# Kernel optimization log

Measured on AMD Instinct MI355X. Metric: run time of the kernel, lower is better.

Reference implementation:

```python
import jax, jax.numpy as jnp
import numpy as np

HIDDEN_DIM = 256
CLIP_LEN = 2
B, NQ, T, D = 64, 10, 2048, 256


def setup_inputs() -> dict:
    key = jax.random.key(0)
    ks = jax.random.split(key, 10)
    s = 1.0 / np.sqrt(HIDDEN_DIM)  # torch GRU/Linear init scale
    return {
        "pred_logits": jax.random.normal(ks[0], (B, NQ, 2), jnp.float32),
        "pred_spans": jax.random.uniform(ks[1], (B, NQ, 2), jnp.float32),
        "memory": jax.random.normal(ks[2], (B, T, D), jnp.float32),
        "src_vid": jax.random.normal(ks[3], (B, T, D), jnp.float32),
        "W_ih": jax.random.normal(ks[4], (3 * D, D), jnp.float32) * s,
        "W_hh": jax.random.normal(ks[5], (3 * D, D), jnp.float32) * s,
        "b_ih": jax.random.normal(ks[6], (3 * D,), jnp.float32) * s,
        "b_hh": jax.random.normal(ks[7], (3 * D,), jnp.float32) * s,
        "W_sal": jax.random.normal(ks[8], (D, D), jnp.float32) * s,
        "b_sal": jax.random.normal(ks[9], (D,), jnp.float32) * s,
    }


def _gru_last_hidden(x, W_ih, W_hh, b_ih, b_hh):
    # x: [B, T, D] -> final hidden state [B, D] (torch nn.GRU, h0 = 0)
    b, t, d = x.shape
    gi = jnp.einsum("btd,gd->btg", x, W_ih) + b_ih  # [B, T, 3D], precompute input gates

    def step(h, gi_t):
        gh = jnp.einsum("bd,gd->bg", h, W_hh) + b_hh
        ir, iz, inn = jnp.split(gi_t, 3, axis=-1)
        hr, hz, hn = jnp.split(gh, 3, axis=-1)
        r = jax.nn.sigmoid(ir + hr)
        z = jax.nn.sigmoid(iz + hz)
        n = jnp.tanh(inn + r * hn)
        h_new = (1.0 - z) * n + z * h
        return h_new, None

    h0 = jnp.zeros((b, d), x.dtype)
    hT, _ = jax.lax.scan(step, h0, jnp.swapaxes(gi, 0, 1))
    return hT


def reference(pred_logits, pred_spans, memory, src_vid, W_ih, W_hh, b_ih, b_hh, W_sal, b_sal):
    b, t, d = memory.shape
    # top-1 span selection (sort descending, take first == argmax of class-0 prob)
    scores = jax.nn.softmax(pred_logits, axis=-1)[..., 0]  # [B, NQ]
    best = jnp.argmax(scores, axis=-1)  # [B]
    span = jnp.take_along_axis(pred_spans, best[:, None, None], axis=1)[:, 0, :]  # [B, 2] (cx, w)
    cx, w = span[:, 0], span[:, 1]
    xx = jnp.stack([cx - 0.5 * w, cx + 0.5 * w], axis=-1) * (t * CLIP_LEN)
    se = jnp.floor(xx / CLIP_LEN).astype(jnp.int32)  # [B, 2] start/end frame indices
    start = jnp.clip(se[:, 0], 0, t - 1)
    end_eff = jnp.minimum(se[:, 1], t - 1)
    # on-device dynamic slice + zero pad to fixed length T (replaces python loop)
    idx = start[:, None] + jnp.arange(t)[None, :]  # [B, T]
    valid = idx <= end_eff[:, None]  # empty slice if end < start
    idx_c = jnp.clip(idx, 0, t - 1)
    sliced = jnp.take_along_axis(src_vid, idx_c[..., None], axis=1) * valid[..., None].astype(src_vid.dtype)
    # GRU over padded slice, take last hidden
    hidden = _gru_last_hidden(sliced, W_ih, W_hh, b_ih, b_hh)  # [B, D]
    weight = jnp.einsum("bd,btd->bt", hidden, src_vid)  # [B, T]
    mem = memory * weight[..., None] + memory
    proj = jnp.einsum("btd,ed->bte", mem, W_sal) + b_sal
    saliency = jnp.sum(proj, axis=-1) / np.sqrt(HIDDEN_DIM)
    return saliency  # [B, T]
```

## Files before the change

kernel.cpp:

```cpp
#include <hip/hip_runtime.h>
#include <hip/hip_bf16.h>
#include <stdint.h>

#define T_SEQ 2048
#define DDIM 256
#define G3 768
#define NB 64
#define NQR 10

typedef _Float16 h2f __attribute__((ext_vector_type(2)));
typedef _Float16 f16x8 __attribute__((ext_vector_type(8)));
typedef float f32x4 __attribute__((ext_vector_type(4)));
typedef unsigned u32x4 __attribute__((ext_vector_type(4)));

__device__ __forceinline__ float fdot2u(unsigned a, unsigned b, float c) {
    return __builtin_amdgcn_fdot2(__builtin_bit_cast(h2f, a),
                                  __builtin_bit_cast(h2f, b), c, false);
}
__device__ __forceinline__ unsigned packf16(float a, float b) {
    auto p = __builtin_amdgcn_cvt_pkrtz(a, b);
    return __builtin_bit_cast(unsigned, p);
}
__device__ __forceinline__ float unpk(unsigned u, int hi) {
    h2f p = __builtin_bit_cast(h2f, u);
    return hi ? (float)p[1] : (float)p[0];
}
__device__ __forceinline__ float sigmf(float x) { return 1.0f / (1.0f + __expf(-x)); }
__device__ __forceinline__ float tanhff(float x) {
    float ax = fabsf(x);
    float e = __expf(2.0f * ax);
    float t = 1.0f - 2.0f / (e + 1.0f);
    return copysignf(t, x);
}

__global__ __launch_bounds__(256) void k_prologue(
    const float* __restrict__ logits, const float* __restrict__ spans,
    const float* __restrict__ W_sal, const float* __restrict__ b_sal,
    int* __restrict__ meta, float* __restrict__ wcol, float* __restrict__ bsum) {
    int tid = threadIdx.x;
    if (tid < NB) {
        int b = tid;
        float bestv = -1e30f; int best = 0;
        for (int q = 0; q < NQR; ++q) {
            float l0 = logits[(b * NQR + q) * 2 + 0];
            float l1 = logits[(b * NQR + q) * 2 + 1];
            float sc = sigmf(l0 - l1);
            if (sc > bestv) { bestv = sc; best = q; }
        }
        float cx = spans[(b * NQR + best) * 2 + 0];
        float w  = spans[(b * NQR + best) * 2 + 1];
        float x0 = (cx - 0.5f * w) * (float)(T_SEQ * 2);
        float x1 = (cx + 0.5f * w) * (float)(T_SEQ * 2);
        int se0 = (int)floorf(x0 * 0.5f);
        int se1 = (int)floorf(x1 * 0.5f);
        int start = min(max(se0, 0), T_SEQ - 1);
        int end_eff = min(se1, T_SEQ - 1);
        int len = end_eff - start + 1;
        if (len < 0) len = 0;
        meta[b] = start; meta[NB + b] = len;
    }
    float acc = 0.f;
    for (int e = 0; e < DDIM; ++e) acc += W_sal[e * DDIM + tid];
    wcol[tid] = acc;
    if (tid < 64) {
        float p = b_sal[tid] + b_sal[tid + 64] + b_sal[tid + 128] + b_sal[tid + 192];
        for (int off = 32; off; off >>= 1) p += __shfl_down(p, off, 64);
        if (tid == 0) *bsum = p;
    }
}

__global__ __launch_bounds__(256) void k_prep(
    const float* __restrict__ W_hh, unsigned* __restrict__ w4) {
    int g = blockIdx.x, k = threadIdx.x;
    if (k < 128) {
        unsigned v = packf16(W_hh[g * DDIM + 2 * k], W_hh[g * DDIM + 2 * k + 1]);
        w4[((k >> 2) * G3 + g) * 4 + (k & 3)] = v;
    }
}

__global__ __launch_bounds__(256) void k_prepI(
    const float* __restrict__ W_ih, unsigned* __restrict__ wfragI) {
    int u = blockIdx.x * 256 + threadIdx.x;
    int jj = u & 3;
    int l  = (u >> 2) & 63;
    int kc = (u >> 8) & 7;
    int ct = u >> 11;
    int col = ct * 16 + (l & 15);
    int k = kc * 32 + ((l >> 4) << 3) + jj * 2;
    wfragI[u] = packf16(W_ih[col * DDIM + k], W_ih[col * DDIM + k + 1]);
}

__global__ __launch_bounds__(512, 2) void k_gemm(
    const float* __restrict__ src_vid, const unsigned* __restrict__ wfragI,
    const float* __restrict__ b_ih, const int* __restrict__ meta,
    unsigned* __restrict__ gi2, int t0, int tc, int TC) {
    int b = blockIdx.y;
    int len = meta[NB + b];
    int start = meta[b];
    int tbase = t0 + blockIdx.x * 256;
    int tend = t0 + tc; if (tend > len) tend = len;
    int tcap = tbase + 256; if (tend > tcap) tend = tcap;
    if (tbase >= tend) return;

    int tid = threadIdx.x, lane = tid & 63, w = tid >> 6;

    u32x4 bfr[6][8];
    const u32x4* wf = (const u32x4*)wfragI;
#pragma unroll
    for (int j = 0; j < 6; ++j)
#pragma unroll
        for (int kc = 0; kc < 8; ++kc)
            bfr[j][kc] = wf[((w * 6 + j) * 8 + kc) * 64 + lane];

    int row = lane & 15, kg = lane >> 4;
    float bv[6];
#pragma unroll
    for (int j = 0; j < 6; ++j) bv[j] = b_ih[(w * 6 + j) * 16 + row];

    __shared__ unsigned As[2048];
    int sr = tid >> 5, sx = tid & 31;

    for (int tch = tbase; tch < tend; tch += 16) {
        int tr = tch + sr;
        u32x4 pk = {0u, 0u, 0u, 0u};
        if (tr < len) {
            const float* sp = src_vid + ((size_t)b * T_SEQ + start + tr) * DDIM + sx * 8;
            float4 a0 = *(const float4*)sp;
            float4 a1 = *(const float4*)(sp + 4);
            pk[0] = packf16(a0.x, a0.y); pk[1] = packf16(a0.z, a0.w);
            pk[2] = packf16(a1.x, a1.y); pk[3] = packf16(a1.z, a1.w);
        }
        *(u32x4*)&As[sr * 128 + ((sx ^ sr) << 2)] = pk;
        __syncthreads();

        f32x4 d[6];
#pragma unroll
        for (int j = 0; j < 6; ++j) d[j] = (f32x4){bv[j], bv[j], bv[j], bv[j]};
#pragma unroll
        for (int kc = 0; kc < 8; ++kc) {
            u32x4 av = *(const u32x4*)&As[row * 128 + (((kc * 4 + kg) ^ row) << 2)];
            f16x8 af = __builtin_bit_cast(f16x8, av);
#pragma unroll
            for (int j = 0; j < 6; ++j)
                d[j] = __builtin_amdgcn_mfma_f32_16x16x32_f16(
                    af, __builtin_bit_cast(f16x8, bfr[j][kc]), d[j], 0, 0, 0);
        }

#pragma unroll
        for (int j = 0; j < 6; ++j) {
            int cflat = (w * 6 + j) * 16 + row;
            int gate = cflat >> 8;
            int pairi = (cflat & 255) >> 1;
#pragma unroll
            for (int reg = 0; reg < 4; ++reg) {
                int t = tch + kg * 4 + reg;
                float v = d[j][reg];
                float o = __shfl_xor(v, 1, 64);
                if (!(lane & 1) && t < tend)
                    gi2[((size_t)b * TC + (t - t0)) * 384 + gate * 128 + pairi] =
                        packf16(v, o);
            }
        }
        __syncthreads();
    }
}

__global__ void __launch_bounds__(512, 2) k_gru(
    const unsigned* __restrict__ gi2, const unsigned* __restrict__ w4,
    const float* __restrict__ b_ih, const float* __restrict__ b_hh,
    const int* __restrict__ meta, float* __restrict__ h_state,
    int t0, int t1, int TC) {
    int b = blockIdx.x, tid = threadIdx.x;
    int c = tid & 255, half = tid >> 8;
    int len = meta[NB + b];

    u32x4 wrq[16], wzq[16], wnq[16];
    const u32x4* w4v = (const u32x4*)w4;
    const u32x4* wb = w4v + (size_t)(half * 16) * G3;
#pragma unroll
    for (int q = 0; q < 16; ++q) {
        wrq[q] = wb[q * G3 + c];
        wzq[q] = wb[q * G3 + 256 + c];
        wnq[q] = wb[q * G3 + 512 + c];
    }

    float bhR = (half == 0) ? b_hh[c] : 0.f;
    float bhZ = (half == 0) ? b_hh[256 + c] : 0.f;
    float bhN = (half == 0) ? b_hh[512 + c] : 0.f;
    float biR = b_ih[c], biZ = b_ih[256 + c], biN = b_ih[512 + c];

    __shared__ unsigned hl[128];
    __shared__ float pl[3][256];

    float h = 0.f;
    if (half == 0) {
        if (t0 != 0) h = h_state[b * DDIM + c];
        float hp = __shfl_xor(h, 1, 64);
        if (!(c & 1)) hl[c >> 1] = packf16(h, hp);
    }

    const unsigned* gb2 = gi2 + (size_t)b * TC * 384 + (c >> 1);
    int sel = c & 1;
    float gR = biR, gZ = biZ, gN = biN;
    if (half == 0 && t0 < t1 && t0 < len) {
        gR = unpk(gb2[0], sel); gZ = unpk(gb2[128], sel); gN = unpk(gb2[256], sel);
    }
    __syncthreads();

    for (int t = t0; t < t1; ++t) {
        float nR = biR, nZ = biZ, nN = biN;
        int tn = t + 1;
        if (half == 0 && tn < t1 && tn < len) {
            const unsigned* gp = gb2 + (size_t)(tn - t0) * 384;
            nR = unpk(gp[0], sel); nZ = unpk(gp[128], sel); nN = unpk(gp[256], sel);
        }
        float r0 = bhR, z0 = bhZ, n0 = bhN, r1 = 0.f, z1 = 0.f, n1 = 0.f;
        const u32x4* hb = (const u32x4*)hl + half * 16;
#pragma unroll
        for (int q = 0; q < 16; ++q) {
            u32x4 h4 = hb[q];
            r0 = fdot2u(h4.x, wrq[q].x, r0);
            z0 = fdot2u(h4.x, wzq[q].x, z0);
            n0 = fdot2u(h4.x, wnq[q].x, n0);
            r1 = fdot2u(h4.y, wrq[q].y, r1);
            z1 = fdot2u(h4.y, wzq[q].y, z1);
            n1 = fdot2u(h4.y, wnq[q].y, n1);
            r0 = fdot2u(h4.z, wrq[q].z, r0);
            z0 = fdot2u(h4.z, wzq[q].z, z0);
            n0 = fdot2u(h4.z, wnq[q].z, n0);
            r1 = fdot2u(h4.w, wrq[q].w, r1);
            z1 = fdot2u(h4.w, wzq[q].w, z1);
            n1 = fdot2u(h4.w, wnq[q].w, n1);
        }
        float hr = r0 + r1, hz = z0 + z1, hn = n0 + n1;
        if (half == 1) {
            pl[0][c] = hr; pl[1][c] = hz; pl[2][c] = hn;
        }
        __syncthreads();
        if (half == 0) {
            hr += pl[0][c]; hz += pl[1][c]; hn += pl[2][c];
            float r = sigmf(gR + hr);
            float z = sigmf(gZ + hz);
            float n = tanhff(gN + r * hn);
            h = (1.0f - z) * n + z * h;
            float hp = __shfl_xor(h, 1, 64);
            if (!(c & 1)) hl[c >> 1] = packf16(h, hp);
        }
        gR = nR; gZ = nZ; gN = nN;
        __syncthreads();
    }
    if (half == 0) h_state[b * DDIM + c] = h;
}

__global__ __launch_bounds__(256) void k_epi(
    const float* __restrict__ memory, const float* __restrict__ src_vid,
    const float* __restrict__ h_state, const float* __restrict__ wcol,
    const float* __restrict__ bsum, float* __restrict__ out) {
    int wid = blockIdx.x * 4 + (threadIdx.x >> 6);
    int lane = threadIdx.x & 63;
    int b = wid >> 11;
    int t = wid & 2047;
    const float4* mp = (const float4*)(memory + ((size_t)b * T_SEQ + t) * DDIM);
    const float4* sp = (const float4*)(src_vid + ((size_t)b * T_SEQ + t) * DDIM);
    const float4* hp = (const float4*)(h_state + b * DDIM);
    const float4* wp = (const float4*)wcol;
    float4 m = mp[lane], s = sp[lane], hv = hp[lane], wc = wp[lane];
    float s1 = m.x * wc.x + m.y * wc.y + m.z * wc.z + m.w * wc.w;
    float s2 = hv.x * s.x + hv.y * s.y + hv.z * s.z + hv.w * s.w;
    for (int off = 32; off; off >>= 1) {
        s1 += __shfl_down(s1, off, 64);
        s2 += __shfl_down(s2, off, 64);
    }
    if (lane == 0) out[(size_t)b * T_SEQ + t] = ((1.0f + s2) * s1 + *bsum) * 0.0625f;
}

extern "C" void kernel_launch(void* const* d_in, const int* in_sizes, int n_in,
                              void* d_out, int out_size, void* d_ws, size_t ws_size,
                              hipStream_t stream) {
    const float* logits  = (const float*)d_in[0];
    const float* spans   = (const float*)d_in[1];
    const float* memory  = (const float*)d_in[2];
    const float* src_vid = (const float*)d_in[3];
    const float* W_ih    = (const float*)d_in[4];
    const float* W_hh    = (const float*)d_in[5];
    const float* b_ih    = (const float*)d_in[6];
    const float* b_hh    = (const float*)d_in[7];
    const float* W_sal   = (const float*)d_in[8];
    const float* b_sal   = (const float*)d_in[9];
    float* out = (float*)d_out;
    char* ws = (char*)d_ws;

    const size_t OFF_META = 0;
    const size_t OFF_WCOL = 1024;
    const size_t OFF_BSUM = 2048;
    const size_t OFF_H    = 4096;
    const size_t OFF_W4   = 69632;
    const size_t OFF_WFI  = 462848;
    const size_t OFF_GI   = 856064;

    int* meta       = (int*)(ws + OFF_META);
    float* wcol     = (float*)(ws + OFF_WCOL);
    float* bsum     = (float*)(ws + OFF_BSUM);
    float* h_state  = (float*)(ws + OFF_H);
    unsigned* w4    = (unsigned*)(ws + OFF_W4);
    unsigned* wfragI= (unsigned*)(ws + OFF_WFI);
    unsigned* gi2   = (unsigned*)(ws + OFF_GI);

    size_t gi_cap = (ws_size > OFF_GI) ? (ws_size - OFF_GI) : 0;
    long long tc_max = (long long)(gi_cap / ((size_t)NB * 384 * 4));
    int TC = (tc_max > T_SEQ) ? T_SEQ : (int)tc_max;
    if (TC < 16) TC = 16;

    k_prologue<<<dim3(1), dim3(256), 0, stream>>>(logits, spans, W_sal, b_sal, meta, wcol, bsum);
    k_prep<<<dim3(G3), dim3(256), 0, stream>>>(W_hh, w4);
    k_prepI<<<dim3(384), dim3(256), 0, stream>>>(W_ih, wfragI);
    for (int t0 = 0; t0 < T_SEQ; t0 += TC) {
        int tc = T_SEQ - t0; if (tc > TC) tc = TC;
        k_gemm<<<dim3((tc + 255) / 256, NB), dim3(512), 0, stream>>>(
            src_vid, wfragI, b_ih, meta, gi2, t0, tc, TC);
        k_gru<<<dim3(NB), dim3(512), 0, stream>>>(
            gi2, w4, b_ih, b_hh, meta, h_state, t0, t0 + tc, TC);
    }
    k_epi<<<dim3(NB * T_SEQ / 4), dim3(256), 0, stream>>>(
        memory, src_vid, h_state, wcol, bsum, out);
}
```

Measured before the change: 2.572 ms.

## Split GRU recurrence K-dimension over four thread groups and fold biases into gates

The GRU recurrent kernel now runs 1024 threads per batch row, splitting the 256-wide hidden dot products across four K-quarters instead of two. Each thread holds only 24 weight vectors instead of 48, and three of the groups reduce their partial sums through shared memory. Input and hidden biases for the r and z gates are pre-combined in the prologue and folded into the input-gate GEMM output, with packed biases used for padded timesteps. The aim is a shorter per-step serial dot-product chain and lower register pressure on the latency-bound recurrence, at the cost of more shared-memory traffic and a larger block per step.

Measured after the change: 2.992 ms. 1.16x slower.

```diff
diff --git a/kernel.cpp b/kernel.cpp
--- a/kernel.cpp
+++ b/kernel.cpp
@@ -36,7 +36,9 @@
 __global__ __launch_bounds__(256) void k_prologue(
     const float* __restrict__ logits, const float* __restrict__ spans,
     const float* __restrict__ W_sal, const float* __restrict__ b_sal,
-    int* __restrict__ meta, float* __restrict__ wcol, float* __restrict__ bsum) {
+    const float* __restrict__ b_ih, const float* __restrict__ b_hh,
+    int* __restrict__ meta, float* __restrict__ wcol, float* __restrict__ bsum,
+    float* __restrict__ bias_comb, unsigned* __restrict__ biasp) {
     int tid = threadIdx.x;
     if (tid < NB) {
         int b = tid;
@@ -67,6 +69,17 @@
         for (int off = 32; off; off >>= 1) p += __shfl_down(p, off, 64);
         if (tid == 0) *bsum = p;
     }
+#pragma unroll
+    for (int r = 0; r < 3; ++r) {
+        int g = tid + r * 256;
+        bias_comb[g] = b_ih[g] + (g < 512 ? b_hh[g] : 0.f);
+    }
+    __syncthreads();
+#pragma unroll
+    for (int r = 0; r < 2; ++r) {
+        int p = tid + r * 256;
+        if (p < 384) biasp[p] = packf16(bias_comb[2 * p], bias_comb[2 * p + 1]);
+    }
 }
 
 __global__ __launch_bounds__(256) void k_prep(
@@ -92,7 +105,7 @@
 
 __global__ __launch_bounds__(512, 2) void k_gemm(
     const float* __restrict__ src_vid, const unsigned* __restrict__ wfragI,
-    const float* __restrict__ b_ih, const int* __restrict__ meta,
+    const float* __restrict__ bias_comb, const int* __restrict__ meta,
     unsigned* __restrict__ gi2, int t0, int tc, int TC) {
     int b = blockIdx.y;
     int len = meta[NB + b];
@@ -115,7 +128,7 @@
     int row = lane & 15, kg = lane >> 4;
     float bv[6];
 #pragma unroll
-    for (int j = 0; j < 6; ++j) bv[j] = b_ih[(w * 6 + j) * 16 + row];
+    for (int j = 0; j < 6; ++j) bv[j] = bias_comb[(w * 6 + j) * 16 + row];
 
     __shared__ unsigned As[2048];
     int sr = tid >> 5, sx = tid & 31;
@@ -165,35 +178,33 @@
     }
 }
 
-__global__ void __launch_bounds__(512, 2) k_gru(
+__global__ void __launch_bounds__(1024) k_gru(
     const unsigned* __restrict__ gi2, const unsigned* __restrict__ w4,
-    const float* __restrict__ b_ih, const float* __restrict__ b_hh,
+    const unsigned* __restrict__ biasp, const float* __restrict__ b_hh,
     const int* __restrict__ meta, float* __restrict__ h_state,
     int t0, int t1, int TC) {
     int b = blockIdx.x, tid = threadIdx.x;
-    int c = tid & 255, half = tid >> 8;
+    int c = tid & 255, kq = tid >> 8;
     int len = meta[NB + b];
 
-    u32x4 wrq[16], wzq[16], wnq[16];
+    u32x4 wq[8][3];
     const u32x4* w4v = (const u32x4*)w4;
-    const u32x4* wb = w4v + (size_t)(half * 16) * G3;
-#pragma unroll
-    for (int q = 0; q < 16; ++q) {
-        wrq[q] = wb[q * G3 + c];
-        wzq[q] = wb[q * G3 + 256 + c];
-        wnq[q] = wb[q * G3 + 512 + c];
-    }
-
-    float bhR = (half == 0) ? b_hh[c] : 0.f;
-    float bhZ = (half == 0) ? b_hh[256 + c] : 0.f;
-    float bhN = (half == 0) ? b_hh[512 + c] : 0.f;
-    float biR = b_ih[c], biZ = b_ih[256 + c], biN = b_ih[512 + c];
+#pragma unroll
+    for (int q = 0; q < 8; ++q)
+#pragma unroll
+        for (int g = 0; g < 3; ++g)
+            wq[q][g] = w4v[(size_t)(kq * 8 + q) * G3 + g * 256 + c];
+
+    float bhN = b_hh[512 + c];
 
     __shared__ unsigned hl[128];
-    __shared__ float pl[3][256];
+    __shared__ float pl[9][256];
+    __shared__ unsigned bias2[384];
+
+    if (tid < 384) bias2[tid] = biasp[tid];
 
     float h = 0.f;
-    if (half == 0) {
+    if (kq == 0) {
         if (t0 != 0) h = h_state[b * DDIM + c];
         float hp = __shfl_xor(h, 1, 64);
         if (!(c & 1)) hl[c >> 1] = packf16(h, hp);
@@ -201,55 +212,71 @@
 
     const unsigned* gb2 = gi2 + (size_t)b * TC * 384 + (c >> 1);
     int sel = c & 1;
-    float gR = biR, gZ = biZ, gN = biN;
-    if (half == 0 && t0 < t1 && t0 < len) {
-        gR = unpk(gb2[0], sel); gZ = unpk(gb2[128], sel); gN = unpk(gb2[256], sel);
-    }
+    float gR = 0.f, gZ = 0.f, gN = 0.f;
     __syncthreads();
+    if (kq == 0 && t0 < t1) {
+        if (t0 < len) {
+            gR = unpk(gb2[0], sel); gZ = unpk(gb2[128], sel); gN = unpk(gb2[256], sel);
+        } else {
+            gR = unpk(bias2[c >> 1], sel);
+            gZ = unpk(bias2[128 + (c >> 1)], sel);
+            gN = unpk(bias2[256 + (c >> 1)], sel);
+        }
+    }
 
     for (int t = t0; t < t1; ++t) {
-        float nR = biR, nZ = biZ, nN = biN;
+        float nR = 0.f, nZ = 0.f, nN = 0.f;
         int tn = t + 1;
-        if (half == 0 && tn < t1 && tn < len) {
-            const unsigned* gp = gb2 + (size_t)(tn - t0) * 384;
-            nR = unpk(gp[0], sel); nZ = unpk(gp[128], sel); nN = unpk(gp[256], sel);
-        }
-        float r0 = bhR, z0 = bhZ, n0 = bhN, r1 = 0.f, z1 = 0.f, n1 = 0.f;
-        const u32x4* hb = (const u32x4*)hl + half * 16;
-#pragma unroll
-        for (int q = 0; q < 16; ++q) {
-            u32x4 h4 = hb[q];
-            r0 = fdot2u(h4.x, wrq[q].x, r0);
-            z0 = fdot2u(h4.x, wzq[q].x, z0);
-            n0 = fdot2u(h4.x, wnq[q].x, n0);
-            r1 = fdot2u(h4.y, wrq[q].y, r1);
-            z1 = fdot2u(h4.y, wzq[q].y, z1);
-            n1 = fdot2u(h4.y, wnq[q].y, n1);
-            r0 = fdot2u(h4.z, wrq[q].z, r0);
-            z0 = fdot2u(h4.z, wzq[q].z, z0);
-            n0 = fdot2u(h4.z, wnq[q].z, n0);
-            r1 = fdot2u(h4.w, wrq[q].w, r1);
-            z1 = fdot2u(h4.w, wzq[q].w, z1);
-            n1 = fdot2u(h4.w, wnq[q].w, n1);
-        }
-        float hr = r0 + r1, hz = z0 + z1, hn = n0 + n1;
-        if (half == 1) {
-            pl[0][c] = hr; pl[1][c] = hz; pl[2][c] = hn;
+        if (kq == 0 && tn < t1) {
+            if (tn < len) {
+                const unsigned* gp = gb2 + (size_t)(tn - t0) * 384;
+                nR = unpk(gp[0], sel); nZ = unpk(gp[128], sel); nN = unpk(gp[256], sel);
+            } else {
+                nR = unpk(bias2[c >> 1], sel);
+                nZ = unpk(bias2[128 + (c >> 1)], sel);
+                nN = unpk(bias2[256 + (c >> 1)], sel);
+            }
+        }
+        float a00 = 0.f, a01 = 0.f, a10 = 0.f, a11 = 0.f, a20 = 0.f, a21 = 0.f;
+        const u32x4* hb = (const u32x4*)hl + kq * 8;
+#pragma unroll
+        for (int q = 0; q < 8; ++q) {
+            u32x4 hq = hb[q];
+            a00 = fdot2u(hq.x, wq[q][0].x, a00);
+            a10 = fdot2u(hq.x, wq[q][1].x, a10);
+            a20 = fdot2u(hq.x, wq[q][2].x, a20);
+            a01 = fdot2u(hq.y, wq[q][0].y, a01);
+            a11 = fdot2u(hq.y, wq[q][1].y, a11);
+            a21 = fdot2u(hq.y, wq[q][2].y, a21);
+            a00 = fdot2u(hq.z, wq[q][0].z, a00);
+            a10 = fdot2u(hq.z, wq[q][1].z, a10);
+            a20 = fdot2u(hq.z, wq[q][2].z, a20);
+            a01 = fdot2u(hq.w, wq[q][0].w, a01);
+            a11 = fdot2u(hq.w, wq[q][1].w, a11);
+            a21 = fdot2u(hq.w, wq[q][2].w, a21);
+        }
+        float s0 = a00 + a01, s1 = a10 + a11, s2 = a20 + a21;
+        if (kq > 0) {
+            pl[(kq - 1) * 3 + 0][c] = s0;
+            pl[(kq - 1) * 3 + 1][c] = s1;
+            pl[(kq - 1) * 3 + 2][c] = s2;
         }
         __syncthreads();
-        if (half == 0) {
-            hr += pl[0][c]; hz += pl[1][c]; hn += pl[2][c];
+        if (kq == 0) {
+            float hr = s0 + pl[0][c] + pl[3][c] + pl[6][c];
+            float hz = s1 + pl[1][c] + pl[4][c] + pl[7][c];
+            float hn = s2 + pl[2][c] + pl[5][c] + pl[8][c];
             float r = sigmf(gR + hr);
             float z = sigmf(gZ + hz);
-            float n = tanhff(gN + r * hn);
+            float n = tanhff(gN + r * (hn + bhN));
             h = (1.0f - z) * n + z * h;
             float hp = __shfl_xor(h, 1, 64);
             if (!(c & 1)) hl[c >> 1] = packf16(h, hp);
-        }
-        gR = nR; gZ = nZ; gN = nN;
+            gR = nR; gZ = nZ; gN = nN;
+        }
         __syncthreads();
     }
-    if (half == 0) h_state[b * DDIM + c] = h;
+    if (kq == 0) h_state[b * DDIM + c] = h;
 }
 
 __global__ __launch_bounds__(256) void k_epi(
@@ -290,36 +317,41 @@
     float* out = (float*)d_out;
     char* ws = (char*)d_ws;
 
-    const size_t OFF_META = 0;
-    const size_t OFF_WCOL = 1024;
-    const size_t OFF_BSUM = 2048;
-    const size_t OFF_H    = 4096;
-    const size_t OFF_W4   = 69632;
-    const size_t OFF_WFI  = 462848;
-    const size_t OFF_GI   = 856064;
-
-    int* meta       = (int*)(ws + OFF_META);
-    float* wcol     = (float*)(ws + OFF_WCOL);
-    float* bsum     = (float*)(ws + OFF_BSUM);
-    float* h_state  = (float*)(ws + OFF_H);
-    unsigned* w4    = (unsigned*)(ws + OFF_W4);
-    unsigned* wfragI= (unsigned*)(ws + OFF_WFI);
-    unsigned* gi2   = (unsigned*)(ws + OFF_GI);
+    const size_t OFF_META  = 0;
+    const size_t OFF_WCOL  = 1024;
+    const size_t OFF_BSUM  = 2048;
+    const size_t OFF_BIASC = 2560;
+    const size_t OFF_BIASP = 5632;
+    const size_t OFF_H     = 8192;
+    const size_t OFF_W4    = 73728;
+    const size_t OFF_WFI   = 466944;
+    const size_t OFF_GI    = 860160;
+
+    int* meta        = (int*)(ws + OFF_META);
+    float* wcol      = (float*)(ws + OFF_WCOL);
+    float* bsum      = (float*)(ws + OFF_BSUM);
+    float* bias_comb = (float*)(ws + OFF_BIASC);
+    unsigned* biasp  = (unsigned*)(ws + OFF_BIASP);
+    float* h_state   = (float*)(ws + OFF_H);
+    unsigned* w4     = (unsigned*)(ws + OFF_W4);
+    unsigned* wfragI = (unsigned*)(ws + OFF_WFI);
+    unsigned* gi2    = (unsigned*)(ws + OFF_GI);
 
     size_t gi_cap = (ws_size > OFF_GI) ? (ws_size - OFF_GI) : 0;
     long long tc_max = (long long)(gi_cap / ((size_t)NB * 384 * 4));
     int TC = (tc_max > T_SEQ) ? T_SEQ : (int)tc_max;
     if (TC < 16) TC = 16;
 
-    k_prologue<<<dim3(1), dim3(256), 0, stream>>>(logits, spans, W_sal, b_sal, meta, wcol, bsum);
+    k_prologue<<<dim3(1), dim3(256), 0, stream>>>(
+        logits, spans, W_sal, b_sal, b_ih, b_hh, meta, wcol, bsum, bias_comb, biasp);
     k_prep<<<dim3(G3), dim3(256), 0, stream>>>(W_hh, w4);
     k_prepI<<<dim3(384), dim3(256), 0, stream>>>(W_ih, wfragI);
     for (int t0 = 0; t0 < T_SEQ; t0 += TC) {
         int tc = T_SEQ - t0; if (tc > TC) tc = TC;
         k_gemm<<<dim3((tc + 255) / 256, NB), dim3(512), 0, stream>>>(
-            src_vid, wfragI, b_ih, meta, gi2, t0, tc, TC);
-        k_gru<<<dim3(NB), dim3(512), 0, stream>>>(
-            gi2, w4, b_ih, b_hh, meta, h_state, t0, t0 + tc, TC);
+            src_vid, wfragI, bias_comb, meta, gi2, t0, tc, TC);
+        k_gru<<<dim3(NB), dim3(1024), 0, stream>>>(
+            gi2, w4, biasp, b_hh, meta, h_state, t0, t0 + tc, TC);
     }
     k_epi<<<dim3(NB * T_SEQ / 4), dim3(256), 0, stream>>>(
         memory, src_vid, h_state, wcol, bsum, out);
```
